# Kernel optimization log

Hardware: AMD Instinct MI355X
Metric: run time of the kernel (lower is better)

## Reference

```python
import jax, jax.numpy as jnp
import numpy as np

EPS = 1e-12  # torch F.normalize default eps


def setup_inputs() -> dict:
    key = jax.random.key(0)
    k1, k2, k3 = jax.random.split(key, 3)
    b, c, H, W = 16, 384, 48, 48
    heads = 8
    x = jax.random.normal(k1, (b, c, H, W), dtype=jnp.float32)
    # torch Linear weight init scale ~ 1/sqrt(fan_in); use scaled normals
    w_qkv = jax.random.normal(k2, (c, 3 * c), dtype=jnp.float32) / np.sqrt(c)
    temperature = jnp.ones((1, heads, 1, 1), dtype=jnp.float32)
    w_out = jax.random.normal(k3, (c, c), dtype=jnp.float32) / np.sqrt(c)
    b_out = jnp.zeros((c,), dtype=jnp.float32)
    return {"x": x, "w_qkv": w_qkv, "temperature": temperature,
            "w_out": w_out, "b_out": b_out}


def reference(x, w_qkv, temperature, w_out, b_out):
    b, c, H, W = x.shape
    h = temperature.shape[1]
    d = c // h
    n = H * W
    # b c h w -> b n c
    xt = x.reshape(b, c, n).transpose(0, 2, 1)
    qkv = xt @ w_qkv  # [b, n, 3c]
    q, k, v = jnp.split(qkv, 3, axis=-1)
    q = q.reshape(b, n, h, d).transpose(0, 2, 1, 3)  # b h n d
    k = k.reshape(b, n, h, d).transpose(0, 2, 3, 1)  # b h d n
    v = v.reshape(b, n, h, d).transpose(0, 2, 1, 3)  # b h n d
    # L2 normalize over the token axis (n): q over dim=-2, k over dim=-1
    q = q / jnp.maximum(jnp.sqrt(jnp.sum(q * q, axis=-2, keepdims=True)), EPS)
    k = k / jnp.maximum(jnp.sqrt(jnp.sum(k * k, axis=-1, keepdims=True)), EPS)
    k = k * temperature
    # cross-covariance attention over channels: [b, h, d, d]
    attn = jnp.einsum('bhpn,bhnq->bhpq', k, q)
    attn = jax.nn.softmax(attn, axis=-1)
    out = jnp.einsum('bhnp,bhpq->bhnq', v, attn)  # [b, h, n, d]
    out = out.transpose(0, 2, 1, 3).reshape(b, n, c)  # b n (h d)
    out = out @ w_out + b_out
    # b n c -> b c h w
    out = out.transpose(0, 2, 1).reshape(b, c, H, W)
    return out
```

## Files before the change

### kernel.cpp

```cpp
#include <hip/hip_runtime.h>
#include <cstdint>

typedef __attribute__((ext_vector_type(8))) short short8;
typedef __attribute__((ext_vector_type(4))) float f32x4;
typedef unsigned int u32;
typedef unsigned short u16;

#define NTOK 2304
#define CDIM 384

__device__ __forceinline__ u16 f2bf(float f) {
    u32 u = __builtin_bit_cast(u32, f);
    u32 r = (u + 0x7FFFu + ((u >> 16) & 1u)) >> 16;
    return (u16)r;
}
__device__ __forceinline__ float bf2f(u32 h) {
    u32 u = h << 16;
    return __builtin_bit_cast(float, u);
}

__global__ __launch_bounds__(256) void transpose_all(
    const float* __restrict__ x, const float* __restrict__ w_qkv,
    u16* __restrict__ xT, u16* __restrict__ xbf,
    u16* __restrict__ wqkvT, u16* __restrict__ wv)
{
    __shared__ float tile[64][65];
    const int bz = blockIdx.z;
    const float* src; int Csz; char* dT; char* dC; int dcCol0; long dcRowB;
    if (bz < 16) {
        src = x + (long)bz * 384 * 2304; Csz = 2304;
        dT = (char*)(xT + (long)bz * 2304 * 384);
        dC = (char*)(xbf + (long)bz * 384 * 2304);
        dcCol0 = 0; dcRowB = 2304 * 2;
    } else {
        if (blockIdx.x >= 18) return;
        src = w_qkv; Csz = 1152;
        dT = (char*)wqkvT; dC = (char*)wv;
        dcCol0 = 768; dcRowB = 384 * 2;
    }
    const int c0 = blockIdx.x * 64;
    const int k0 = blockIdx.y * 64;
    const int t = threadIdx.x;
    const int rr = t >> 2, cc4 = (t & 3) * 16;

    const float* srow = src + (long)(k0 + rr) * Csz + c0 + cc4;
#pragma unroll
    for (int i = 0; i < 4; ++i) {
        float4 v = *(const float4*)(srow + i * 4);
        tile[rr][cc4 + i*4 + 0] = v.x;
        tile[rr][cc4 + i*4 + 1] = v.y;
        tile[rr][cc4 + i*4 + 2] = v.z;
        tile[rr][cc4 + i*4 + 3] = v.w;
    }
    __syncthreads();

    {
        char* drow = dT + (long)(c0 + rr) * (CDIM * 2);
        const int sw = (rr & 7) << 4;
#pragma unroll
        for (int half = 0; half < 2; ++half) {
            u32 pk[4];
#pragma unroll
            for (int i = 0; i < 4; ++i) {
                float v0 = tile[cc4 + half*8 + 2*i][rr];
                float v1 = tile[cc4 + half*8 + 2*i + 1][rr];
                pk[i] = (u32)f2bf(v0) | ((u32)f2bf(v1) << 16);
            }
            uint4 q; q.x = pk[0]; q.y = pk[1]; q.z = pk[2]; q.w = pk[3];
            const int inrow = (k0 + cc4 + half*8) * 2;
            *(uint4*)(drow + (inrow ^ sw)) = q;
        }
    }
    if (c0 >= dcCol0) {
        char* drow = dC + (long)(k0 + rr) * dcRowB;
        const int sw = (rr & 7) << 4;
#pragma unroll
        for (int half = 0; half < 2; ++half) {
            u32 pk[4];
#pragma unroll
            for (int i = 0; i < 4; ++i) {
                float v0 = tile[rr][cc4 + half*8 + 2*i];
                float v1 = tile[rr][cc4 + half*8 + 2*i + 1];
                pk[i] = (u32)f2bf(v0) | ((u32)f2bf(v1) << 16);
            }
            uint4 q; q.x = pk[0]; q.y = pk[1]; q.z = pk[2]; q.w = pk[3];
            const int inrow = (c0 - dcCol0 + cc4 + half*8) * 2;
            *(uint4*)(drow + (inrow ^ sw)) = q;
        }
    }
}

template<int MODE, int KT, int GX, int GY>
__global__ __launch_bounds__(256) void mfma_gemm(
    const u16* __restrict__ A, long aBatch,
    const u16* __restrict__ Bm, long bBatch,
    void* __restrict__ Ovoid, long oBatch, int ostride,
    const float* __restrict__ bias)
{
    constexpr int KB  = KT * 128;
    constexpr int KE  = KT * 64;
    constexpr int NWG = GX * GY * 16;
    __shared__ __attribute__((aligned(16))) u16 As[2][128 * 64];
    __shared__ __attribute__((aligned(16))) u16 Bs[2][128 * 64];

    const int lid = blockIdx.x + GX * (blockIdx.y + GY * blockIdx.z);
    const int swzid = (lid & 7) * (NWG / 8) + (lid >> 3);
    const int b   = swzid / (GX * GY);
    const int rem = swzid % (GX * GY);
    const int m0 = (rem % GX) * 128, n0 = (rem / GX) * 128;

    const u16* Ab = A + (long)b * aBatch + (long)m0 * KE;
    const u16* Bb = Bm + (long)b * bBatch + (long)n0 * KE;
    const int t = threadIdx.x;
    const int w = t >> 6, l = t & 63;
    const int wm = (w >> 1) * 64, wn = (w & 1) * 64;
    const int srow = t >> 3;
    const int scol = (t & 7) * 16;
    f32x4 acc[4][4] = {};

    auto stage = [&](int buf, int kt) {
        const int kbyte = kt * 128;
#pragma unroll
        for (int i = 0; i < 4; ++i) {
            const int row = srow + i * 32;
            const long so = (long)row * KB + kbyte + scol;
            const int d = (i * 256 + t) * 16;
            __builtin_amdgcn_global_load_lds(
                (const __attribute__((address_space(1))) u32*)((const char*)Ab + so),
                (__attribute__((address_space(3))) u32*)((char*)&As[buf][0] + d), 16, 0, 0);
            __builtin_amdgcn_global_load_lds(
                (const __attribute__((address_space(1))) u32*)((const char*)Bb + so),
                (__attribute__((address_space(3))) u32*)((char*)&Bs[buf][0] + d), 16, 0, 0);
        }
    };

    stage(0, 0);
    __syncthreads();
    int cur = 0;
#pragma unroll 1
    for (int kt = 0; kt < KT; ++kt) {
        if (kt < KT - 1) stage(cur ^ 1, kt + 1);
        const char* Ac = (const char*)&As[cur][0];
        const char* Bc = (const char*)&Bs[cur][0];
#pragma unroll
        for (int kk = 0; kk < 2; ++kk) {
            short8 af[4], bfr[4];
#pragma unroll
            for (int mi = 0; mi < 4; ++mi) {
                const int m = wm + mi * 16 + (l & 15);
                const int off = m * 128 + ((kk * 64 + (l >> 4) * 16) ^ ((m & 7) << 4));
                af[mi] = *(const short8*)(Ac + off);
            }
#pragma unroll
            for (int ni = 0; ni < 4; ++ni) {
                const int n = wn + ni * 16 + (l & 15);
                const int off = n * 128 + ((kk * 64 + (l >> 4) * 16) ^ ((n & 7) << 4));
                bfr[ni] = *(const short8*)(Bc + off);
            }
#pragma unroll
            for (int mi = 0; mi < 4; ++mi)
#pragma unroll
                for (int ni = 0; ni < 4; ++ni)
                    acc[mi][ni] = __builtin_amdgcn_mfma_f32_16x16x32_bf16(
                        af[mi], bfr[ni], acc[mi][ni], 0, 0, 0);
        }
        __syncthreads();
        cur ^= 1;
    }

    if (MODE == 0) {
        u16* O = (u16*)Ovoid + (long)b * oBatch;
#pragma unroll
        for (int mi = 0; mi < 4; ++mi) {
            const int mb = m0 + wm + mi * 16 + (l >> 4) * 4;
#pragma unroll
            for (int ni = 0; ni < 4; ++ni) {
                const int n = n0 + wn + ni * 16 + (l & 15);
#pragma unroll
                for (int r = 0; r < 4; ++r)
                    O[(long)(mb + r) * ostride + n] = f2bf(acc[mi][ni][r]);
            }
        }
    } else if (MODE == 1) {
        float* O = (float*)Ovoid + (long)b * oBatch;
#pragma unroll
        for (int mi = 0; mi < 4; ++mi) {
            const int mb = m0 + wm + mi * 16 + (l >> 4) * 4;
#pragma unroll
            for (int r = 0; r < 4; ++r) {
                const float bb = bias[mb + r];
#pragma unroll
                for (int ni = 0; ni < 4; ++ni) {
                    const int n = n0 + wn + ni * 16 + (l & 15);
                    O[(long)(mb + r) * ostride + n] = acc[mi][ni][r] + bb;
                }
            }
        }
    } else {
        char* Ob = (char*)Ovoid + (long)b * oBatch * 2;
#pragma unroll
        for (int mi = 0; mi < 4; ++mi) {
            const int mb = m0 + wm + mi * 16 + (l >> 4) * 4;
#pragma unroll
            for (int ni = 0; ni < 4; ++ni) {
                const int n = n0 + wn + ni * 16 + (l & 15);
#pragma unroll
                for (int r = 0; r < 4; ++r) {
                    const int m = mb + r;
                    const long byteoff = (long)m * (ostride * 2) +
                        (((long)n * 2) ^ ((m & 7) << 4));
                    *(u16*)(Ob + byteoff) = f2bf(acc[mi][ni][r]);
                }
            }
        }
    }
}

__global__ __launch_bounds__(256) void s_softmax(
    const u16* __restrict__ Tp,
    const u16* __restrict__ wT,
    const float* __restrict__ temp, float* __restrict__ Sbuf)
{
    __shared__ float Sp[4][48][48];
    __shared__ float S[48][49];
    __shared__ float invk[48], invq[48];
    const int h = blockIdx.x, b = blockIdx.y, t = threadIdx.x;
    const int w = t >> 6, l = t & 63, lr = l & 15, lk = (l >> 4) * 8;

    const u16* Tk = Tp + ((long)b * 768 + 384 + h * 48) * CDIM;
    f32x4 acc[3][3] = {};
#pragma unroll
    for (int ks = 0; ks < 3; ++ks) {
        const int k0 = w * 96 + ks * 32 + lk;
        short8 af[3], bfr[3];
#pragma unroll
        for (int mi = 0; mi < 3; ++mi)
            af[mi] = *(const short8*)(Tk + (long)(mi * 16 + lr) * CDIM + k0);
#pragma unroll
        for (int ni = 0; ni < 3; ++ni) {
            const int row = h * 48 + ni * 16 + lr;
            const char* base = (const char*)wT + (long)row * 768;
            bfr[ni] = *(const short8*)(base + ((k0 * 2) ^ ((row & 7) << 4)));
        }
#pragma unroll
        for (int mi = 0; mi < 3; ++mi)
#pragma unroll
            for (int ni = 0; ni < 3; ++ni)
                acc[mi][ni] = __builtin_amdgcn_mfma_f32_16x16x32_bf16(
                    af[mi], bfr[ni], acc[mi][ni], 0, 0, 0);
    }
#pragma unroll
    for (int mi = 0; mi < 3; ++mi)
#pragma unroll
        for (int ni = 0; ni < 3; ++ni)
#pragma unroll
            for (int r = 0; r < 4; ++r)
                Sp[w][mi * 16 + (l >> 4) * 4 + r][ni * 16 + lr] = acc[mi][ni][r];
    if (t < 96) {
        const int ch = (t < 48) ? (h * 48 + t) : (384 + h * 48 + (t - 48));
        const u16* trow = Tp + ((long)b * 768 + ch) * CDIM;
        const char* wrow = (const char*)wT + (long)ch * 768;
        const int sw = (ch & 7) << 4;
        float s = 0.f;
#pragma unroll 4
        for (int i = 0; i < 48; ++i) {
            short8 tv = *(const short8*)(trow + i * 8);
            short8 wv = *(const short8*)(wrow + ((i * 16) ^ sw));
#pragma unroll
            for (int e = 0; e < 8; ++e)
                s += bf2f((u16)tv[e]) * bf2f((u16)wv[e]);
        }
        float inv = 1.0f / fmaxf(sqrtf(fmaxf(s, 0.f)), 1e-12f);
        if (t < 48) invq[t] = inv; else invk[t - 48] = inv;
    }
    __syncthreads();
    for (int idx = t; idx < 2304; idx += 256) {
        const int p = idx / 48, q = idx % 48;
        S[p][q] = Sp[0][p][q] + Sp[1][p][q] + Sp[2][p][q] + Sp[3][p][q];
    }
    __syncthreads();
    if (t < 48) {
        const float sc = temp[h] * invk[t];
        float row[48];
        float mx = -1e30f;
#pragma unroll 8
        for (int q = 0; q < 48; ++q) {
            row[q] = S[t][q] * sc * invq[q];
            mx = fmaxf(mx, row[q]);
        }
        float ssum = 0.f;
#pragma unroll 8
        for (int q = 0; q < 48; ++q) {
            row[q] = __expf(row[q] - mx);
            ssum += row[q];
        }
        float inv = 1.0f / ssum;
#pragma unroll 8
        for (int q = 0; q < 48; ++q) S[t][q] = row[q] * inv;
    }
    __syncthreads();
    float* sp = Sbuf + (long)(b * 8 + h) * 2304;
    for (int idx = t; idx < 2304; idx += 256)
        sp[idx] = S[idx / 48][idx % 48];
}

__global__ __launch_bounds__(256) void fold_gemm(
    const float* __restrict__ Sbuf, const float* __restrict__ w_out,
    u16* __restrict__ W2T)
{
    __shared__ float Sl[48][49];
    __shared__ float wl[48][68];
    const int jt = blockIdx.x, h = blockIdx.y, b = blockIdx.z;
    const int t = threadIdx.x;
    const int j0 = jt * 64;
    const float* sp = Sbuf + (long)(b * 8 + h) * 2304;
    for (int idx = t; idx < 2304; idx += 256)
        Sl[idx / 48][idx % 48] = sp[idx];
#pragma unroll
    for (int i = 0; i < 3; ++i) {
        int idx = t + i * 256;
        int q = idx >> 4, c4 = (idx & 15) * 4;
        float4 v = *(const float4*)(w_out + (long)(h * 48 + q) * 384 + j0 + c4);
        *(float4*)&wl[q][c4] = v;
    }
    __syncthreads();
    u16* Wb = W2T + (long)b * 384 * 384;
#pragma unroll
    for (int pass = 0; pass < 2; ++pass) {
        const int wi = t + pass * 256;
        if (wi < 384) {
            const int j = wi & 63, pg = wi >> 6;
            float s[8] = {};
#pragma unroll
            for (int q = 0; q < 48; ++q) {
                float wv = wl[q][j];
#pragma unroll
                for (int i = 0; i < 8; ++i) s[i] += Sl[pg * 8 + i][q] * wv;
            }
            u32 pk[4];
#pragma unroll
            for (int i = 0; i < 4; ++i)
                pk[i] = (u32)f2bf(s[2 * i]) | ((u32)f2bf(s[2 * i + 1]) << 16);
            const int jg = j0 + j;
            const int byteoff = jg * 768 +
                (((h * 48 + pg * 8) * 2) ^ ((jg & 7) << 4));
            uint4 qv; qv.x = pk[0]; qv.y = pk[1]; qv.z = pk[2]; qv.w = pk[3];
            *(uint4*)((char*)Wb + byteoff) = qv;
        }
    }
}

extern "C" void kernel_launch(void* const* d_in, const int* in_sizes, int n_in,
                              void* d_out, int out_size, void* d_ws, size_t ws_size,
                              hipStream_t stream) {
    const float* x     = (const float*)d_in[0];
    const float* w_qkv = (const float*)d_in[1];
    const float* temp  = (const float*)d_in[2];
    const float* w_out = (const float*)d_in[3];
    const float* b_out = (const float*)d_in[4];
    float* out = (float*)d_out;

    char* ws = (char*)d_ws;
    const size_t SZ_XBF = 16UL * 384 * 2304 * 2;
    const size_t SZ_XT  = 16UL * 2304 * 384 * 2;
    const size_t SZ_WQT = 1152UL * 384 * 2;
    const size_t SZ_WV  = 384UL * 384 * 2;
    const size_t SZ_G   = 16UL * 384 * 384 * 2;
    const size_t SZ_TP  = 16UL * 768 * 384 * 2;
    const size_t SZ_SB  = 16UL * 8 * 2304 * 4;
    const size_t SZ_W2  = 16UL * 384 * 384 * 2;

    size_t off = 0;
    u16*   xbf   = (u16*)(ws + off); off += SZ_XBF;
    u16*   xT    = (u16*)(ws + off); off += SZ_XT;
    u16*   wqkvT = (u16*)(ws + off); off += SZ_WQT;
    u16*   wv    = (u16*)(ws + off); off += SZ_WV;
    u16*   Gs    = (u16*)(ws + off); off += SZ_G;
    u16*   Tp    = (u16*)(ws + off); off += SZ_TP;
    float* Sbuf  = (float*)(ws + off); off += SZ_SB;
    u16*   W2T   = (u16*)(ws + off); off += SZ_W2;
    u16*   W3    = (u16*)(ws + off);

    transpose_all<<<dim3(36, 6, 17), 256, 0, stream>>>(
        x, w_qkv, xT, xbf, wqkvT, wv);
    mfma_gemm<2, 36, 3, 3><<<dim3(3, 3, 16), 256, 0, stream>>>(
        xbf, 384L * 2304, xbf, 384L * 2304, Gs, 384L * 384, 384, nullptr);
    mfma_gemm<0, 6, 6, 3><<<dim3(6, 3, 16), 256, 0, stream>>>(
        wqkvT, 0L, Gs, 384L * 384, Tp, 768L * 384, 384, nullptr);
    s_softmax<<<dim3(8, 16), 256, 0, stream>>>(Tp, wqkvT, temp, Sbuf);
    fold_gemm<<<dim3(6, 8, 16), 256, 0, stream>>>(Sbuf, w_out, W2T);
    mfma_gemm<2, 6, 3, 3><<<dim3(3, 3, 16), 256, 0, stream>>>(
        W2T, 384L * 384, wv, 0L, W3, 384L * 384, 384, nullptr);
    mfma_gemm<1, 6, 3, 18><<<dim3(3, 18, 16), 256, 0, stream>>>(
        W3, 384L * 384, xT, 384L * 2304, out, 384L * 2304, 2304, b_out);
}
```

Measured before the change: 129.8 us.

## Fuse fp32 load into Gram GEMM and merge softmax with MFMA fold

The Gram-matrix GEMM now reads fp32 x directly, converting to bf16 while staging into LDS, so the transpose kernel no longer writes a bf16 copy of x and that intermediate buffer is removed. The softmax kernel is merged with the fold step: it writes the normalized attention to LDS as bf16 and multiplies it by a pre-transposed bf16 w_out using MFMA. This replaces the separate scalar fp32 fold kernel and its fp32 Sbuf round trip. The cost is extra per-tile conversion work in the Gram GEMM, which is a 3x3x16 grid with 36 K-steps, and bf16 rounding of the softmax output before the fold.

```diff
diff --git a/kernel.cpp b/kernel.cpp
--- a/kernel.cpp
+++ b/kernel.cpp
@@ -21,22 +21,25 @@
 
 __global__ __launch_bounds__(256) void transpose_all(
     const float* __restrict__ x, const float* __restrict__ w_qkv,
-    u16* __restrict__ xT, u16* __restrict__ xbf,
-    u16* __restrict__ wqkvT, u16* __restrict__ wv)
+    const float* __restrict__ w_out,
+    u16* __restrict__ xT, u16* __restrict__ wqkvT,
+    u16* __restrict__ wv, u16* __restrict__ woutT)
 {
     __shared__ float tile[64][65];
     const int bz = blockIdx.z;
-    const float* src; int Csz; char* dT; char* dC; int dcCol0; long dcRowB;
+    const float* src; int Csz; char* dT; char* dC = nullptr;
+    int dcCol0 = 0; long dcRowB = 0; bool doC = false;
     if (bz < 16) {
         src = x + (long)bz * 384 * 2304; Csz = 2304;
         dT = (char*)(xT + (long)bz * 2304 * 384);
-        dC = (char*)(xbf + (long)bz * 384 * 2304);
-        dcCol0 = 0; dcRowB = 2304 * 2;
-    } else {
+    } else if (bz == 16) {
         if (blockIdx.x >= 18) return;
         src = w_qkv; Csz = 1152;
-        dT = (char*)wqkvT; dC = (char*)wv;
-        dcCol0 = 768; dcRowB = 384 * 2;
+        dT = (char*)wqkvT; dC = (char*)wv; dcCol0 = 768; dcRowB = 768; doC = true;
+    } else {
+        if (blockIdx.x >= 6) return;
+        src = w_out; Csz = 384;
+        dT = (char*)woutT;
     }
     const int c0 = blockIdx.x * 64;
     const int k0 = blockIdx.y * 64;
@@ -71,7 +74,7 @@
             *(uint4*)(drow + (inrow ^ sw)) = q;
         }
     }
-    if (c0 >= dcCol0) {
+    if (doC && c0 >= dcCol0) {
         char* drow = dC + (long)(k0 + rr) * dcRowB;
         const int sw = (rr & 7) << 4;
 #pragma unroll
@@ -86,6 +89,110 @@
             uint4 q; q.x = pk[0]; q.y = pk[1]; q.z = pk[2]; q.w = pk[3];
             const int inrow = (c0 - dcCol0 + cc4 + half*8) * 2;
             *(uint4*)(drow + (inrow ^ sw)) = q;
+        }
+    }
+}
+
+__global__ __launch_bounds__(256) void g_gemm(
+    const float* __restrict__ x, u16* __restrict__ Gs)
+{
+    __shared__ __attribute__((aligned(16))) u16 As[2][128 * 64];
+    __shared__ __attribute__((aligned(16))) u16 Bs[2][128 * 64];
+    const int lid = blockIdx.x + 3 * (blockIdx.y + 3 * blockIdx.z);
+    const int swzid = (lid & 7) * 18 + (lid >> 3);
+    const int b = swzid / 9, rem = swzid % 9;
+    const int m0 = (rem % 3) * 128, n0 = (rem / 3) * 128;
+    const float* xb = x + (long)b * 384 * NTOK;
+
+    const int t = threadIdx.x;
+    const int w = t >> 6, l = t & 63;
+    const int wm = (w >> 1) * 64, wn = (w & 1) * 64;
+    const int rbase = t >> 3;
+    const int col8 = (t & 7) * 8;
+    const int wbyte = (t & 7) * 16;
+
+    f32x4 acc[4][4] = {};
+    float4 ra[8], rb[8];
+
+    auto issue = [&](int kt) {
+        const float* pa = xb + (long)(m0 + rbase) * NTOK + kt * 64 + col8;
+        const float* pb = xb + (long)(n0 + rbase) * NTOK + kt * 64 + col8;
+#pragma unroll
+        for (int i = 0; i < 4; ++i) {
+            ra[2*i]   = *(const float4*)(pa + (long)(32 * i) * NTOK);
+            ra[2*i+1] = *(const float4*)(pa + (long)(32 * i) * NTOK + 4);
+            rb[2*i]   = *(const float4*)(pb + (long)(32 * i) * NTOK);
+            rb[2*i+1] = *(const float4*)(pb + (long)(32 * i) * NTOK + 4);
+        }
+    };
+    auto cvtwrite = [&](int buf) {
+#pragma unroll
+        for (int i = 0; i < 4; ++i) {
+            const int r = rbase + 32 * i;
+            const int off = r * 128 + (wbyte ^ ((r & 7) << 4));
+            uint4 qa, qb;
+            qa.x = (u32)f2bf(ra[2*i].x)   | ((u32)f2bf(ra[2*i].y)   << 16);
+            qa.y = (u32)f2bf(ra[2*i].z)   | ((u32)f2bf(ra[2*i].w)   << 16);
+            qa.z = (u32)f2bf(ra[2*i+1].x) | ((u32)f2bf(ra[2*i+1].y) << 16);
+            qa.w = (u32)f2bf(ra[2*i+1].z) | ((u32)f2bf(ra[2*i+1].w) << 16);
+            qb.x = (u32)f2bf(rb[2*i].x)   | ((u32)f2bf(rb[2*i].y)   << 16);
+            qb.y = (u32)f2bf(rb[2*i].z)   | ((u32)f2bf(rb[2*i].w)   << 16);
+            qb.z = (u32)f2bf(rb[2*i+1].x) | ((u32)f2bf(rb[2*i+1].y) << 16);
+            qb.w = (u32)f2bf(rb[2*i+1].z) | ((u32)f2bf(rb[2*i+1].w) << 16);
+            *(uint4*)((char*)&As[buf][0] + off) = qa;
+            *(uint4*)((char*)&Bs[buf][0] + off) = qb;
+        }
+    };
+
+    issue(0);
+    cvtwrite(0);
+    __syncthreads();
+    int cur = 0;
+#pragma unroll 1
+    for (int kt = 0; kt < 36; ++kt) {
+        if (kt < 35) issue(kt + 1);
+        const char* Ac = (const char*)&As[cur][0];
+        const char* Bc = (const char*)&Bs[cur][0];
+#pragma unroll
+        for (int kk = 0; kk < 2; ++kk) {
+            short8 af[4], bfr[4];
+#pragma unroll
+            for (int mi = 0; mi < 4; ++mi) {
+                const int m = wm + mi * 16 + (l & 15);
+                const int off = m * 128 + ((kk * 64 + (l >> 4) * 16) ^ ((m & 7) << 4));
+                af[mi] = *(const short8*)(Ac + off);
+            }
+#pragma unroll
+            for (int ni = 0; ni < 4; ++ni) {
+                const int n = wn + ni * 16 + (l & 15);
+                const int off = n * 128 + ((kk * 64 + (l >> 4) * 16) ^ ((n & 7) << 4));
+                bfr[ni] = *(const short8*)(Bc + off);
+            }
+#pragma unroll
+            for (int mi = 0; mi < 4; ++mi)
+#pragma unroll
+                for (int ni = 0; ni < 4; ++ni)
+                    acc[mi][ni] = __builtin_amdgcn_mfma_f32_16x16x32_bf16(
+                        af[mi], bfr[ni], acc[mi][ni], 0, 0, 0);
+        }
+        if (kt < 35) cvtwrite(cur ^ 1);
+        __syncthreads();
+        cur ^= 1;
+    }
+
+    char* Ob = (char*)Gs + (long)b * 294912;
+#pragma unroll
+    for (int mi = 0; mi < 4; ++mi) {
+        const int mb = m0 + wm + mi * 16 + (l >> 4) * 4;
+#pragma unroll
+        for (int ni = 0; ni < 4; ++ni) {
+            const int n = n0 + wn + ni * 16 + (l & 15);
+#pragma unroll
+            for (int r = 0; r < 4; ++r) {
+                const int m = mb + r;
+                const long byteoff = (long)m * 768 + (((long)n * 2) ^ ((m & 7) << 4));
+                *(u16*)(Ob + byteoff) = f2bf(acc[mi][ni][r]);
+            }
         }
     }
 }
@@ -216,48 +323,54 @@
     }
 }
 
-__global__ __launch_bounds__(256) void s_softmax(
+__global__ __launch_bounds__(256) void sm_fold(
     const u16* __restrict__ Tp,
     const u16* __restrict__ wT,
-    const float* __restrict__ temp, float* __restrict__ Sbuf)
+    const float* __restrict__ temp,
+    const u16* __restrict__ woutT,
+    u16* __restrict__ W2T)
 {
     __shared__ float Sp[4][48][48];
     __shared__ float S[48][49];
     __shared__ float invk[48], invq[48];
+    __shared__ __attribute__((aligned(16))) u16 Sbf[48 * 64];
     const int h = blockIdx.x, b = blockIdx.y, t = threadIdx.x;
     const int w = t >> 6, l = t & 63, lr = l & 15, lk = (l >> 4) * 8;
-
-    const u16* Tk = Tp + ((long)b * 768 + 384 + h * 48) * CDIM;
-    f32x4 acc[3][3] = {};
-#pragma unroll
-    for (int ks = 0; ks < 3; ++ks) {
-        const int k0 = w * 96 + ks * 32 + lk;
-        short8 af[3], bfr[3];
+    const int h48 = h * 48;
+
+    const u16* Tk = Tp + ((long)b * 768 + 384 + h48) * CDIM;
+    {
+        f32x4 acc[3][3] = {};
+#pragma unroll
+        for (int ks = 0; ks < 3; ++ks) {
+            const int k0 = w * 96 + ks * 32 + lk;
+            short8 af[3], bfr[3];
+#pragma unroll
+            for (int mi = 0; mi < 3; ++mi)
+                af[mi] = *(const short8*)(Tk + (long)(mi * 16 + lr) * CDIM + k0);
+#pragma unroll
+            for (int ni = 0; ni < 3; ++ni) {
+                const int row = h48 + ni * 16 + lr;
+                const char* base = (const char*)wT + (long)row * 768;
+                bfr[ni] = *(const short8*)(base + ((k0 * 2) ^ ((row & 7) << 4)));
+            }
+#pragma unroll
+            for (int mi = 0; mi < 3; ++mi)
+#pragma unroll
+                for (int ni = 0; ni < 3; ++ni)
+                    acc[mi][ni] = __builtin_amdgcn_mfma_f32_16x16x32_bf16(
+                        af[mi], bfr[ni], acc[mi][ni], 0, 0, 0);
+        }
 #pragma unroll
         for (int mi = 0; mi < 3; ++mi)
-            af[mi] = *(const short8*)(Tk + (long)(mi * 16 + lr) * CDIM + k0);
-#pragma unroll
-        for (int ni = 0; ni < 3; ++ni) {
-            const int row = h * 48 + ni * 16 + lr;
-            const char* base = (const char*)wT + (long)row * 768;
-            bfr[ni] = *(const short8*)(base + ((k0 * 2) ^ ((row & 7) << 4)));
-        }
-#pragma unroll
-        for (int mi = 0; mi < 3; ++mi)
 #pragma unroll
             for (int ni = 0; ni < 3; ++ni)
-                acc[mi][ni] = __builtin_amdgcn_mfma_f32_16x16x32_bf16(
-                    af[mi], bfr[ni], acc[mi][ni], 0, 0, 0);
-    }
-#pragma unroll
-    for (int mi = 0; mi < 3; ++mi)
-#pragma unroll
-        for (int ni = 0; ni < 3; ++ni)
-#pragma unroll
-            for (int r = 0; r < 4; ++r)
-                Sp[w][mi * 16 + (l >> 4) * 4 + r][ni * 16 + lr] = acc[mi][ni][r];
+#pragma unroll
+                for (int r = 0; r < 4; ++r)
+                    Sp[w][mi * 16 + (l >> 4) * 4 + r][ni * 16 + lr] = acc[mi][ni][r];
+    }
     if (t < 96) {
-        const int ch = (t < 48) ? (h * 48 + t) : (384 + h * 48 + (t - 48));
+        const int ch = (t < 48) ? (h48 + t) : (384 + h48 + (t - 48));
         const u16* trow = Tp + ((long)b * 768 + ch) * CDIM;
         const char* wrow = (const char*)wT + (long)ch * 768;
         const int sw = (ch & 7) << 4;
@@ -295,58 +408,62 @@
             ssum += row[q];
         }
         float inv = 1.0f / ssum;
-#pragma unroll 8
-        for (int q = 0; q < 48; ++q) S[t][q] = row[q] * inv;
+        const int sw = (t & 7) << 4;
+#pragma unroll
+        for (int g = 0; g < 8; ++g) {
+            u32 pk[4];
+#pragma unroll
+            for (int e = 0; e < 4; ++e) {
+                const int q0 = g * 8 + 2 * e;
+                float v0 = (q0 < 48) ? row[q0] * inv : 0.f;
+                float v1 = (q0 + 1 < 48) ? row[q0 + 1] * inv : 0.f;
+                pk[e] = (u32)f2bf(v0) | ((u32)f2bf(v1) << 16);
+            }
+            uint4 qv; qv.x = pk[0]; qv.y = pk[1]; qv.z = pk[2]; qv.w = pk[3];
+            *(uint4*)((char*)Sbf + t * 128 + ((g * 16) ^ sw)) = qv;
+        }
     }
     __syncthreads();
-    float* sp = Sbuf + (long)(b * 8 + h) * 2304;
-    for (int idx = t; idx < 2304; idx += 256)
-        sp[idx] = S[idx / 48][idx % 48];
-}
-
-__global__ __launch_bounds__(256) void fold_gemm(
-    const float* __restrict__ Sbuf, const float* __restrict__ w_out,
-    u16* __restrict__ W2T)
-{
-    __shared__ float Sl[48][49];
-    __shared__ float wl[48][68];
-    const int jt = blockIdx.x, h = blockIdx.y, b = blockIdx.z;
-    const int t = threadIdx.x;
-    const int j0 = jt * 64;
-    const float* sp = Sbuf + (long)(b * 8 + h) * 2304;
-    for (int idx = t; idx < 2304; idx += 256)
-        Sl[idx / 48][idx % 48] = sp[idx];
-#pragma unroll
-    for (int i = 0; i < 3; ++i) {
-        int idx = t + i * 256;
-        int q = idx >> 4, c4 = (idx & 15) * 4;
-        float4 v = *(const float4*)(w_out + (long)(h * 48 + q) * 384 + j0 + c4);
-        *(float4*)&wl[q][c4] = v;
-    }
-    __syncthreads();
-    u16* Wb = W2T + (long)b * 384 * 384;
-#pragma unroll
-    for (int pass = 0; pass < 2; ++pass) {
-        const int wi = t + pass * 256;
-        if (wi < 384) {
-            const int j = wi & 63, pg = wi >> 6;
-            float s[8] = {};
-#pragma unroll
-            for (int q = 0; q < 48; ++q) {
-                float wv = wl[q][j];
-#pragma unroll
-                for (int i = 0; i < 8; ++i) s[i] += Sl[pg * 8 + i][q] * wv;
-            }
-            u32 pk[4];
-#pragma unroll
-            for (int i = 0; i < 4; ++i)
-                pk[i] = (u32)f2bf(s[2 * i]) | ((u32)f2bf(s[2 * i + 1]) << 16);
-            const int jg = j0 + j;
-            const int byteoff = jg * 768 +
-                (((h * 48 + pg * 8) * 2) ^ ((jg & 7) << 4));
-            uint4 qv; qv.x = pk[0]; qv.y = pk[1]; qv.z = pk[2]; qv.w = pk[3];
-            *(uint4*)((char*)Wb + byteoff) = qv;
-        }
+    {
+        const char* SbfB = (const char*)Sbf;
+        const int jw = w * 96;
+        f32x4 fac[3][6] = {};
+#pragma unroll
+        for (int ks = 0; ks < 2; ++ks) {
+            const int ka = ks * 64 + (l >> 4) * 16;
+            const int kb = h * 96 + ka;
+            short8 af[3], bfr[6];
+#pragma unroll
+            for (int mi = 0; mi < 3; ++mi) {
+                const int p = mi * 16 + lr;
+                af[mi] = *(const short8*)(SbfB + p * 128 + (ka ^ ((p & 7) << 4)));
+            }
+#pragma unroll
+            for (int ni = 0; ni < 6; ++ni) {
+                const int j = jw + ni * 16 + lr;
+                bfr[ni] = *(const short8*)((const char*)woutT + (long)j * 768 +
+                                           (kb ^ ((j & 7) << 4)));
+            }
+#pragma unroll
+            for (int mi = 0; mi < 3; ++mi)
+#pragma unroll
+                for (int ni = 0; ni < 6; ++ni)
+                    fac[mi][ni] = __builtin_amdgcn_mfma_f32_16x16x32_bf16(
+                        af[mi], bfr[ni], fac[mi][ni], 0, 0, 0);
+        }
+        char* Wb = (char*)W2T + (long)b * 294912;
+#pragma unroll
+        for (int mi = 0; mi < 3; ++mi)
+#pragma unroll
+            for (int ni = 0; ni < 6; ++ni)
+#pragma unroll
+                for (int r = 0; r < 4; ++r) {
+                    const int p = mi * 16 + (l >> 4) * 4 + r;
+                    const int j = jw + ni * 16 + lr;
+                    const long byteoff = (long)j * 768 +
+                        (((h48 + p) * 2) ^ ((j & 7) << 4));
+                    *(u16*)(Wb + byteoff) = f2bf(fac[mi][ni][r]);
+                }
     }
 }
 
@@ -361,34 +478,30 @@
     float* out = (float*)d_out;
 
     char* ws = (char*)d_ws;
-    const size_t SZ_XBF = 16UL * 384 * 2304 * 2;
     const size_t SZ_XT  = 16UL * 2304 * 384 * 2;
     const size_t SZ_WQT = 1152UL * 384 * 2;
     const size_t SZ_WV  = 384UL * 384 * 2;
+    const size_t SZ_WOT = 384UL * 384 * 2 + 256;
     const size_t SZ_G   = 16UL * 384 * 384 * 2;
     const size_t SZ_TP  = 16UL * 768 * 384 * 2;
-    const size_t SZ_SB  = 16UL * 8 * 2304 * 4;
     const size_t SZ_W2  = 16UL * 384 * 384 * 2;
 
     size_t off = 0;
-    u16*   xbf   = (u16*)(ws + off); off += SZ_XBF;
-    u16*   xT    = (u16*)(ws + off); off += SZ_XT;
-    u16*   wqkvT = (u16*)(ws + off); off += SZ_WQT;
-    u16*   wv    = (u16*)(ws + off); off += SZ_WV;
-    u16*   Gs    = (u16*)(ws + off); off += SZ_G;
-    u16*   Tp    = (u16*)(ws + off); off += SZ_TP;
-    float* Sbuf  = (float*)(ws + off); off += SZ_SB;
-    u16*   W2T   = (u16*)(ws + off); off += SZ_W2;
-    u16*   W3    = (u16*)(ws + off);
-
-    transpose_all<<<dim3(36, 6, 17), 256, 0, stream>>>(
-        x, w_qkv, xT, xbf, wqkvT, wv);
-    mfma_gemm<2, 36, 3, 3><<<dim3(3, 3, 16), 256, 0, stream>>>(
-        xbf, 384L * 2304, xbf, 384L * 2304, Gs, 384L * 384, 384, nullptr);
+    u16* xT    = (u16*)(ws + off); off += SZ_XT;
+    u16* wqkvT = (u16*)(ws + off); off += SZ_WQT;
+    u16* wv    = (u16*)(ws + off); off += SZ_WV;
+    u16* woutT = (u16*)(ws + off); off += SZ_WOT;
+    u16* Gs    = (u16*)(ws + off); off += SZ_G;
+    u16* Tp    = (u16*)(ws + off); off += SZ_TP;
+    u16* W2T   = (u16*)(ws + off); off += SZ_W2;
+    u16* W3    = (u16*)(ws + off);
+
+    transpose_all<<<dim3(36, 6, 18), 256, 0, stream>>>(
+        x, w_qkv, w_out, xT, wqkvT, wv, woutT);
+    g_gemm<<<dim3(3, 3, 16), 256, 0, stream>>>(x, Gs);
     mfma_gemm<0, 6, 6, 3><<<dim3(6, 3, 16), 256, 0, stream>>>(
         wqkvT, 0L, Gs, 384L * 384, Tp, 768L * 384, 384, nullptr);
-    s_softmax<<<dim3(8, 16), 256, 0, stream>>>(Tp, wqkvT, temp, Sbuf);
-    fold_gemm<<<dim3(6, 8, 16), 256, 0, stream>>>(Sbuf, w_out, W2T);
+    sm_fold<<<dim3(8, 16), 256, 0, stream>>>(Tp, wqkvT, temp, woutT, W2T);
     mfma_gemm<2, 6, 3, 3><<<dim3(3, 3, 16), 256, 0, stream>>>(
         W2T, 384L * 384, wv, 0L, W3, 384L * 384, 384, nullptr);
     mfma_gemm<1, 6, 3, 18><<<dim3(3, 18, 16), 256, 0, stream>>>(
```

After: 151.1 us. 16.5% more time.
